# Performance work log

Hardware: AMD Instinct MI355X
Metric: run time of the kernel (lower is better)

The kernel has to match this reference:

```python
import jax, jax.numpy as jnp
import numpy as np

N, E, D, H, C = 100000, 1600000, 64, 8, 10
NEG_SLOPE = 0.2


def setup_inputs() -> dict:
    key = jax.random.key(0)
    ks = jax.random.split(key, 20)
    rn = lambda k, sh: jax.random.normal(k, sh, jnp.float32) * 0.1
    return dict(
        x=jax.random.normal(ks[0], (N, D), jnp.float32),
        edge_index=jax.random.randint(ks[1], (2, E), 0, N),
        gcnK_W=rn(ks[2], (D, D)), gcnK_b=rn(ks[3], (D,)),
        gcnV_W=rn(ks[4], (D, D)), gcnV_b=rn(ks[5], (D,)),
        super_Q=rn(ks[6], (C, D)),
        mha_in_w=rn(ks[7], (3 * D, D)), mha_in_b=rn(ks[8], (3 * D,)),
        mha_out_w=rn(ks[9], (D, D)), mha_out_b=rn(ks[10], (D,)),
        gat_W=rn(ks[11], (D, D)), gat_Wc=rn(ks[12], (D, D)),
        gat_a_src=rn(ks[13], (D,)), gat_a_dst=rn(ks[14], (D,)),
        gat_b=rn(ks[15], (D,)),
        t1_W=rn(ks[16], (D, 2 * D)), t1_b=rn(ks[17], (2 * D,)),
        t2_W=rn(ks[18], (2 * D, D)), t2_b=rn(ks[19], (D,)),
    )


def _gcn(x, W, b, src, dst, norm_e):
    # PyG GCNConv: symmetric-normalized aggregation over (A + I)
    h = x @ W  # [N, D]
    agg = jax.ops.segment_sum(h[src] * norm_e[:, None], dst, num_segments=N)
    return agg + b


def _mha(q, k, v, in_w, in_b, out_w, out_b):
    # torch.nn.MultiheadAttention (unbatched), eval mode (dropout off)
    L, n, hd = q.shape[0], k.shape[0], D // H
    Wq, Wk, Wv = jnp.split(in_w, 3, axis=0)
    bq, bk, bv = jnp.split(in_b, 3)
    scale = 1.0 / float(np.sqrt(hd))
    qh = ((q @ Wq.T + bq) * scale).reshape(L, H, hd).transpose(1, 0, 2)  # [H,L,hd]
    kh = (k @ Wk.T + bk).reshape(n, H, hd).transpose(1, 0, 2)            # [H,n,hd]
    vh = (v @ Wv.T + bv).reshape(n, H, hd).transpose(1, 0, 2)
    attn = jax.nn.softmax(jnp.einsum('hld,hnd->hln', qh, kh), axis=-1)
    o = jnp.einsum('hln,hnd->hld', attn, vh).transpose(1, 0, 2).reshape(L, D)
    return o @ out_w.T + out_b


def _context_gat(x, src, dst, context, W, Wc, a_src, a_dst, b):
    # context-conditioned GAT: per-edge logits use node terms + global context gate
    h = x @ W
    c = context @ Wc  # [D]
    s_src = h @ (a_src + c)  # context modulates source attention vector
    s_dst = h @ a_dst
    logits = jax.nn.leaky_relu(s_src[src] + s_dst[dst], NEG_SLOPE)  # [E]
    m = jax.ops.segment_max(logits, dst, num_segments=N)
    ex = jnp.exp(logits - m[dst])
    denom = jax.ops.segment_sum(ex, dst, num_segments=N)
    alpha = ex / (denom[dst] + 1e-16)
    out = jax.ops.segment_sum(alpha[:, None] * h[src], dst, num_segments=N)
    return out + b


def reference(x, edge_index, gcnK_W, gcnK_b, gcnV_W, gcnV_b, super_Q,
              mha_in_w, mha_in_b, mha_out_w, mha_out_b,
              gat_W, gat_Wc, gat_a_src, gat_a_dst, gat_b,
              t1_W, t1_b, t2_W, t2_b):
    src, dst = edge_index[0], edge_index[1]
    loop = jnp.arange(N)
    srcl = jnp.concatenate([src, loop])
    dstl = jnp.concatenate([dst, loop])
    deg = jax.ops.segment_sum(jnp.ones_like(srcl, jnp.float32), dstl, num_segments=N)
    dinv = jnp.where(deg > 0, 1.0 / jnp.sqrt(deg), 0.0)
    norm_e = dinv[srcl] * dinv[dstl]
    x_K = _gcn(x, gcnK_W, gcnK_b, srcl, dstl, norm_e)
    x_V = _gcn(x, gcnV_W, gcnV_b, srcl, dstl, norm_e)
    cluster = _mha(super_Q, x_K, x_V, mha_in_w, mha_in_b, mha_out_w, mha_out_b)  # [C, D]
    context = jnp.mean(cluster, axis=0)  # [D]
    g = _context_gat(x_V, src, dst, context, gat_W, gat_Wc, gat_a_src, gat_a_dst, gat_b)
    h1 = jax.nn.relu(g @ t1_W + t1_b)
    return jax.nn.relu(h1 @ t2_W + t2_b)
```

## Files before the change

kernel.cpp:

```cpp
#include <hip/hip_runtime.h>
#include <hip/hip_bf16.h>
#include <stdint.h>

#define NN 100000
#define EE 1600000
#define NBK 391
#define CHUNK 4096
#define NCB 98
#define BPH 128

#define FMA4(xi, vv, a, base)                      \
  a[(base)+0] = fmaf((xi), (vv).x, a[(base)+0]);   \
  a[(base)+1] = fmaf((xi), (vv).y, a[(base)+1]);   \
  a[(base)+2] = fmaf((xi), (vv).z, a[(base)+2]);   \
  a[(base)+3] = fmaf((xi), (vv).w, a[(base)+3]);

__device__ inline unsigned pack_bf2(float a, float b) {
  __hip_bfloat162 t;
  t.x = __float2bfloat16(a);
  t.y = __float2bfloat16(b);
  return *reinterpret_cast<unsigned*>(&t);
}

__launch_bounds__(256)
__global__ void k_hist(const int* __restrict__ ei, int* __restrict__ histmat) {
  __shared__ int hist[NCB];
  int t = threadIdx.x;
  if (t < NCB) hist[t] = 0;
  __syncthreads();
  int base = blockIdx.x * CHUNK;
  int nb = EE - base; if (nb > CHUNK) nb = CHUNK;
  for (int k = t; k < nb; k += 256)
    atomicAdd(&hist[ei[EE + base + k] >> 10], 1);
  __syncthreads();
  if (t < NCB) histmat[blockIdx.x * NCB + t] = hist[t];
}

__launch_bounds__(256)
__global__ void k_sumcb(const int* __restrict__ histmat, int* __restrict__ cbsum) {
  __shared__ int red[4];
  int cb = blockIdx.x, t = threadIdx.x;
  int s = 0;
  for (int blk = t; blk < NBK; blk += 256) s += histmat[blk * NCB + cb];
#pragma unroll
  for (int off = 32; off > 0; off >>= 1) s += __shfl_down(s, off);
  if ((t & 63) == 0) red[t >> 6] = s;
  __syncthreads();
  if (t == 0) cbsum[cb] = red[0] + red[1] + red[2] + red[3];
}

__launch_bounds__(128)
__global__ void k_scancb(const int* __restrict__ cbsum, int* __restrict__ bstart,
                         int* __restrict__ offsets) {
  __shared__ int sm[128];
  int t = threadIdx.x;
  int v = (t < NCB) ? cbsum[t] : 0;
  sm[t] = v;
  __syncthreads();
  for (int off = 1; off < 128; off <<= 1) {
    int x = (t >= off) ? sm[t - off] : 0;
    __syncthreads();
    sm[t] += x;
    __syncthreads();
  }
  if (t < NCB) bstart[t] = sm[t] - v;
  if (t == 0) { bstart[NCB] = EE; offsets[NN] = EE; }
}

__launch_bounds__(512)
__global__ void k_ppos(const int* __restrict__ histmat, const int* __restrict__ bstart,
                       int* __restrict__ ppos) {
  __shared__ int sm[512];
  int cb = blockIdx.x, t = threadIdx.x;
  int v = (t < NBK) ? histmat[t * NCB + cb] : 0;
  sm[t] = v;
  __syncthreads();
  for (int off = 1; off < 512; off <<= 1) {
    int x = (t >= off) ? sm[t - off] : 0;
    __syncthreads();
    sm[t] += x;
    __syncthreads();
  }
  if (t < NBK) ppos[cb * NBK + t] = bstart[cb] + sm[t] - v;
}

__launch_bounds__(256)
__global__ void k_fill_b(const int* __restrict__ ei, const int* __restrict__ ppos,
                         unsigned* __restrict__ brec) {
  __shared__ int hist[NCB], binstart[NCB], bincur[NCB], pbase[NCB];
  __shared__ unsigned lbuf[CHUNK];
  __shared__ unsigned char cbArr[CHUNK];
  int t = threadIdx.x;
  int base = blockIdx.x * CHUNK;
  int nb = EE - base; if (nb > CHUNK) nb = CHUNK;
  if (t < NCB) { hist[t] = 0; pbase[t] = ppos[t * NBK + blockIdx.x]; }
  __syncthreads();
  unsigned rec[16]; int rcb[16]; int cnt = 0;
  for (int k = t; k < nb; k += 256) {
    int s = ei[base + k], d = ei[EE + base + k];
    rec[cnt] = (unsigned)s | ((unsigned)(d & 1023) << 17);
    rcb[cnt] = d >> 10;
    atomicAdd(&hist[rcb[cnt]], 1);
    cnt++;
  }
  __syncthreads();
  if (t < NCB) binstart[t] = hist[t];
  __syncthreads();
  for (int off = 1; off < NCB; off <<= 1) {
    int v = (t < NCB && t >= off) ? binstart[t - off] : 0;
    __syncthreads();
    if (t < NCB) binstart[t] += v;
    __syncthreads();
  }
  if (t < NCB) { binstart[t] -= hist[t]; bincur[t] = 0; }
  __syncthreads();
  for (int i = 0; i < cnt; i++) {
    int c = rcb[i];
    int pos = atomicAdd(&bincur[c], 1);
    int p = binstart[c] + pos;
    lbuf[p] = rec[i];
    cbArr[p] = (unsigned char)c;
  }
  __syncthreads();
  for (int i = t; i < nb; i += 256) {
    int c = cbArr[i];
    brec[pbase[c] + (i - binstart[c])] = lbuf[i];
  }
}

__launch_bounds__(1024)
__global__ void k_fill_c(const unsigned* __restrict__ brec, const int* __restrict__ bstart,
                         int* __restrict__ csr, int* __restrict__ offsets,
                         float* __restrict__ dinv) {
  __shared__ int cnt[1024], sm[1024];
  int cbk = blockIdx.x, t = threadIdx.x;
  int nb0 = cbk << 10;
  int nn = NN - nb0; if (nn > 1024) nn = 1024;
  cnt[t] = 0;
  __syncthreads();
  int e0 = bstart[cbk], e1 = bstart[cbk + 1];
  for (int j = e0 + t; j < e1; j += 1024)
    atomicAdd(&cnt[brec[j] >> 17], 1);
  __syncthreads();
  int cv = cnt[t];
  sm[t] = cv;
  __syncthreads();
  for (int off = 1; off < 1024; off <<= 1) {
    int v = (t >= off) ? sm[t - off] : 0;
    __syncthreads();
    sm[t] += v;
    __syncthreads();
  }
  sm[t] -= cv;
  if (t < nn) {
    offsets[nb0 + t] = e0 + sm[t];
    dinv[nb0 + t] = rsqrtf((float)(cv + 1));
  }
  cnt[t] = 0;
  __syncthreads();
  for (int j = e0 + t; j < e1; j += 1024) {
    unsigned r = brec[j];
    int dl = r >> 17;
    int p = atomicAdd(&cnt[dl], 1);
    csr[e0 + sm[dl] + p] = r & 0x1FFFF;
  }
}

__global__ void k_prep(const float* __restrict__ x, const float* __restrict__ dinv,
                       unsigned* __restrict__ xbf2) {
  int i = blockIdx.x * 256 + threadIdx.x;
  if (i >= NN * 32) return;
  float dv = dinv[i >> 5];
  float2 v = ((const float2*)x)[i];
  xbf2[i] = pack_bf2(v.x * dv, v.y * dv);
}

__launch_bounds__(256)
__global__ void k_agg_x(const unsigned* __restrict__ xbf2, const int* __restrict__ offsets,
                        const int* __restrict__ csr, const float* __restrict__ dinv,
                        float* __restrict__ ax) {
  int gid = blockIdx.x * 256 + threadIdx.x;
  int n = gid >> 6;
  if (n >= NN) return;
  int lane = gid & 63, q = lane & 7, grp = lane >> 3;
  int e0 = offsets[n], e1 = offsets[n + 1];
  float dv = dinv[n];
  float a[8];
#pragma unroll
  for (int i = 0; i < 8; i++) a[i] = 0.f;
  if (grp == 0) {
    uint4 u = ((const uint4*)(xbf2 + (size_t)n * 32))[q];
    unsigned uu[4] = {u.x, u.y, u.z, u.w};
#pragma unroll
    for (int p = 0; p < 4; p++) {
      __hip_bfloat162 v = *reinterpret_cast<__hip_bfloat162*>(&uu[p]);
      a[2 * p] += __bfloat162float(v.x);
      a[2 * p + 1] += __bfloat162float(v.y);
    }
  }
  for (int base = e0; base < e1; base += 8) {
    int j = base + grp;
    if (j < e1) {
      int s = csr[j];
      uint4 u = ((const uint4*)(xbf2 + (size_t)s * 32))[q];
      unsigned uu[4] = {u.x, u.y, u.z, u.w};
#pragma unroll
      for (int p = 0; p < 4; p++) {
        __hip_bfloat162 v = *reinterpret_cast<__hip_bfloat162*>(&uu[p]);
        a[2 * p] += __bfloat162float(v.x);
        a[2 * p + 1] += __bfloat162float(v.y);
      }
    }
  }
#pragma unroll
  for (int i = 0; i < 8; i++) {
    a[i] += __shfl_xor(a[i], 8);
    a[i] += __shfl_xor(a[i], 16);
    a[i] += __shfl_xor(a[i], 32);
  }
  if (lane < 8) {
    float4* op = (float4*)(ax + (size_t)n * 64 + q * 8);
    op[0] = make_float4(a[0] * dv, a[1] * dv, a[2] * dv, a[3] * dv);
    op[1] = make_float4(a[4] * dv, a[5] * dv, a[6] * dv, a[7] * dv);
  }
}

__global__ void k_fusew(const float* __restrict__ gcnK_W, const float* __restrict__ gcnK_b,
                        const float* __restrict__ gcnV_W, const float* __restrict__ gcnV_b,
                        const float* __restrict__ mha_in_w, const float* __restrict__ mha_in_b,
                        const float* __restrict__ gat_W,
                        float* __restrict__ Wfk, float* __restrict__ Wfv,
                        float* __restrict__ Wfg, float* __restrict__ bf) {
  int blk = blockIdx.x;
  if (blk < 48) {
    int m = blk >> 4;
    int e = (blk & 15) * 256 + threadIdx.x;
    int i = e >> 6, c = e & 63;
    float s = 0.f;
    if (m == 0) {
      for (int j = 0; j < 64; j++) s = fmaf(gcnK_W[i * 64 + j], mha_in_w[(64 + c) * 64 + j], s);
      Wfk[e] = s;
    } else if (m == 1) {
      for (int j = 0; j < 64; j++) s = fmaf(gcnV_W[i * 64 + j], mha_in_w[(128 + c) * 64 + j], s);
      Wfv[e] = s;
    } else {
      for (int j = 0; j < 64; j++) s = fmaf(gcnV_W[i * 64 + j], gat_W[j * 64 + c], s);
      Wfg[e] = s;
    }
  } else {
    int t = threadIdx.x;
    if (t < 64) {
      float s = mha_in_b[64 + t];
      for (int j = 0; j < 64; j++) s = fmaf(gcnK_b[j], mha_in_w[(64 + t) * 64 + j], s);
      bf[t] = s;
    } else if (t < 128) {
      int c = t - 64;
      float s = mha_in_b[128 + c];
      for (int j = 0; j < 64; j++) s = fmaf(gcnV_b[j], mha_in_w[(128 + c) * 64 + j], s);
      bf[64 + c] = s;
    } else if (t < 192) {
      int c = t - 128;
      float s = 0.f;
      for (int j = 0; j < 64; j++) s = fmaf(gcnV_b[j], gat_W[j * 64 + c], s);
      bf[128 + c] = s;
    }
  }
}

__global__ void k_qh(const float* __restrict__ sQ, const float* __restrict__ in_w,
                     const float* __restrict__ in_b, float* __restrict__ qh) {
  int t = blockIdx.x * 256 + threadIdx.x;
  if (t >= 640) return;
  int l = t >> 6, c = t & 63;
  float acc = 0.f;
  for (int i = 0; i < 64; i++) acc = fmaf(sQ[l * 64 + i], in_w[c * 64 + i], acc);
  qh[t] = (acc + in_b[c]) * 0.35355339059327373f;
}

__launch_bounds__(256)
__global__ void k_proj(const float* __restrict__ ax, const float* __restrict__ Wfk,
                       const float* __restrict__ Wfv, const float* __restrict__ Wfg,
                       const float* __restrict__ bf, const float* __restrict__ a_dst,
                       float* __restrict__ Kh, float* __restrict__ Vh,
                       unsigned* __restrict__ hGb, float* __restrict__ s_dstv) {
  __shared__ float sX[64 * 65];
  __shared__ float sWk[4096], sWv[4096], sWg[4096];
  __shared__ float sB[192], sAd[64];
  int t = threadIdx.x;
  int base = blockIdx.x * 64;
  for (int i = t; i < 4096; i += 256) { sWk[i] = Wfk[i]; sWv[i] = Wfv[i]; sWg[i] = Wfg[i]; }
  if (t < 192) sB[t] = bf[t];
  if (t < 64) sAd[t] = a_dst[t];
  for (int idx = t; idx < 64 * 16; idx += 256) {
    int rl = idx >> 4, k4 = idx & 15;
    int row = base + rl;
    float4 v = (row < NN) ? ((const float4*)ax)[(size_t)row * 16 + k4]
                          : make_float4(0.f, 0.f, 0.f, 0.f);
    sX[rl * 65 + 4 * k4 + 0] = v.x;
    sX[rl * 65 + 4 * k4 + 1] = v.y;
    sX[rl * 65 + 4 * k4 + 2] = v.z;
    sX[rl * 65 + 4 * k4 + 3] = v.w;
  }
  __syncthreads();
  int cg = t & 7, rg = t >> 3;
  int r0 = rg * 2;
  float aK[16], aV[16], aG[16];
#pragma unroll
  for (int i = 0; i < 16; i++) { aK[i] = 0.f; aV[i] = 0.f; aG[i] = 0.f; }
  const float4* Wk4 = (const float4*)sWk;
  const float4* Wv4 = (const float4*)sWv;
  const float4* Wg4 = (const float4*)sWg;
#pragma unroll 2
  for (int i = 0; i < 64; i++) {
    float x0 = sX[r0 * 65 + i];
    float x1 = sX[(r0 + 1) * 65 + i];
    float4 wk0 = Wk4[i * 16 + cg * 2], wk1 = Wk4[i * 16 + cg * 2 + 1];
    float4 wv0 = Wv4[i * 16 + cg * 2], wv1 = Wv4[i * 16 + cg * 2 + 1];
    float4 wg0 = Wg4[i * 16 + cg * 2], wg1 = Wg4[i * 16 + cg * 2 + 1];
    FMA4(x0, wk0, aK, 0); FMA4(x0, wk1, aK, 4);
    FMA4(x1, wk0, aK, 8); FMA4(x1, wk1, aK, 12);
    FMA4(x0, wv0, aV, 0); FMA4(x0, wv1, aV, 4);
    FMA4(x1, wv0, aV, 8); FMA4(x1, wv1, aV, 12);
    FMA4(x0, wg0, aG, 0); FMA4(x0, wg1, aG, 4);
    FMA4(x1, wg0, aG, 8); FMA4(x1, wg1, aG, 12);
  }
#pragma unroll
  for (int r = 0; r < 2; r++) {
    int row = base + r0 + r;
    bool ok = row < NN;
    int o = r * 8;
    float hg[8];
    float sd = 0.f;
#pragma unroll
    for (int c = 0; c < 8; c++) {
      hg[c] = aG[o + c] + sB[128 + cg * 8 + c];
      sd = fmaf(hg[c], sAd[cg * 8 + c], sd);
    }
    sd += __shfl_xor(sd, 1);
    sd += __shfl_xor(sd, 2);
    sd += __shfl_xor(sd, 4);
    if (ok) {
      float4* kp = (float4*)(Kh + (size_t)cg * NN * 8 + (size_t)row * 8);
      kp[0] = make_float4(aK[o + 0] + sB[cg * 8 + 0], aK[o + 1] + sB[cg * 8 + 1],
                          aK[o + 2] + sB[cg * 8 + 2], aK[o + 3] + sB[cg * 8 + 3]);
      kp[1] = make_float4(aK[o + 4] + sB[cg * 8 + 4], aK[o + 5] + sB[cg * 8 + 5],
                          aK[o + 6] + sB[cg * 8 + 6], aK[o + 7] + sB[cg * 8 + 7]);
      float4* vp = (float4*)(Vh + (size_t)cg * NN * 8 + (size_t)row * 8);
      vp[0] = make_float4(aV[o + 0] + sB[64 + cg * 8 + 0], aV[o + 1] + sB[64 + cg * 8 + 1],
                          aV[o + 2] + sB[64 + cg * 8 + 2], aV[o + 3] + sB[64 + cg * 8 + 3]);
      vp[1] = make_float4(aV[o + 4] + sB[64 + cg * 8 + 4], aV[o + 5] + sB[64 + cg * 8 + 5],
                          aV[o + 6] + sB[64 + cg * 8 + 6], aV[o + 7] + sB[64 + cg * 8 + 7]);
      uint4 u;
      u.x = pack_bf2(hg[0], hg[1]);
      u.y = pack_bf2(hg[2], hg[3]);
      u.z = pack_bf2(hg[4], hg[5]);
      u.w = pack_bf2(hg[6], hg[7]);
      ((uint4*)(hGb + (size_t)row * 32))[cg] = u;
      if (cg == 0) s_dstv[row] = sd;
    }
  }
}

__launch_bounds__(256)
__global__ void k_mha(const float* __restrict__ Kh, const float* __restrict__ Vh,
                      const float* __restrict__ qh, float* __restrict__ part) {
  int h = blockIdx.x / BPH, b = blockIdx.x % BPH;
  __shared__ float sq[80];
  __shared__ float red[4][90];
  if (threadIdx.x < 80) {
    int l = threadIdx.x >> 3, j = threadIdx.x & 7;
    sq[threadIdx.x] = qh[l * 64 + h * 8 + j];
  }
  __syncthreads();
  const float4* Kp = (const float4*)(Kh + (size_t)h * NN * 8);
  const float4* Vp = (const float4*)(Vh + (size_t)h * NN * 8);
  const float4* sq4 = (const float4*)sq;
  float s[10], o[80];
#pragma unroll
  for (int l = 0; l < 10; l++) s[l] = 0.f;
#pragma unroll
  for (int t = 0; t < 80; t++) o[t] = 0.f;
  for (int n = b * 256 + threadIdx.x; n < NN; n += BPH * 256) {
    float4 k0 = Kp[n * 2], k1 = Kp[n * 2 + 1];
    float4 v0 = Vp[n * 2], v1 = Vp[n * 2 + 1];
#pragma unroll
    for (int l = 0; l < 10; l++) {
      float4 q0 = sq4[l * 2], q1 = sq4[l * 2 + 1];
      float z = q0.x * k0.x + q0.y * k0.y + q0.z * k0.z + q0.w * k0.w +
                q1.x * k1.x + q1.y * k1.y + q1.z * k1.z + q1.w * k1.w;
      float w = __expf(z);
      s[l] += w;
      o[l * 8 + 0] = fmaf(w, v0.x, o[l * 8 + 0]);
      o[l * 8 + 1] = fmaf(w, v0.y, o[l * 8 + 1]);
      o[l * 8 + 2] = fmaf(w, v0.z, o[l * 8 + 2]);
      o[l * 8 + 3] = fmaf(w, v0.w, o[l * 8 + 3]);
      o[l * 8 + 4] = fmaf(w, v1.x, o[l * 8 + 4]);
      o[l * 8 + 5] = fmaf(w, v1.y, o[l * 8 + 5]);
      o[l * 8 + 6] = fmaf(w, v1.z, o[l * 8 + 6]);
      o[l * 8 + 7] = fmaf(w, v1.w, o[l * 8 + 7]);
    }
  }
  int lane = threadIdx.x & 63, wave = threadIdx.x >> 6;
#pragma unroll
  for (int l = 0; l < 10; l++) {
    float v = s[l];
#pragma unroll
    for (int off = 32; off > 0; off >>= 1) v += __shfl_down(v, off);
    if (lane == 0) red[wave][l] = v;
  }
#pragma unroll
  for (int t = 0; t < 80; t++) {
    float v = o[t];
#pragma unroll
    for (int off = 32; off > 0; off >>= 1) v += __shfl_down(v, off);
    if (lane == 0) red[wave][10 + t] = v;
  }
  __syncthreads();
  if (threadIdx.x < 90) {
    float v = red[0][threadIdx.x] + red[1][threadIdx.x] +
              red[2][threadIdx.x] + red[3][threadIdx.x];
    part[(size_t)blockIdx.x * 90 + threadIdx.x] = v;
  }
}

__global__ void k_mred(const float* __restrict__ part, float* __restrict__ acc) {
  int t = blockIdx.x * 256 + threadIdx.x;
  if (t >= 720) return;
  int h = t / 90, j = t % 90;
  float v = 0.f;
  for (int b = 0; b < BPH; b++) v += part[(size_t)(h * BPH + b) * 90 + j];
  if (j < 10) acc[h * 10 + j] = v;
  else acc[80 + h * 80 + (j - 10)] = v;
}

__global__ void k_context(const float* __restrict__ acc, const float* __restrict__ out_w,
                          const float* __restrict__ out_b, const float* __restrict__ a_src,
                          const float* __restrict__ gat_Wc, float* __restrict__ aeff) {
  __shared__ float po[640], cl[640], ctx[64];
  int t = threadIdx.x;
  {
    int h = t / 80, r = t % 80, l = r >> 3, j = r & 7;
    po[l * 64 + h * 8 + j] = acc[80 + t] / acc[h * 10 + l];
  }
  __syncthreads();
  {
    int l = t >> 6, d = t & 63;
    float v = out_b[d];
    for (int c = 0; c < 64; c++) v = fmaf(po[l * 64 + c], out_w[d * 64 + c], v);
    cl[t] = v;
  }
  __syncthreads();
  if (t < 64) {
    float m = 0.f;
#pragma unroll
    for (int l = 0; l < 10; l++) m += cl[l * 64 + t];
    ctx[t] = m * 0.1f;
  }
  __syncthreads();
  if (t < 64) {
    float v = a_src[t];
    for (int i = 0; i < 64; i++) v = fmaf(ctx[i], gat_Wc[i * 64 + t], v);
    aeff[t] = v;
  }
}

__launch_bounds__(256)
__global__ void k_ssrc(const unsigned* __restrict__ hGb, const float* __restrict__ aeff,
                       float* __restrict__ s_src) {
  int gid = blockIdx.x * 256 + threadIdx.x;
  int n = gid >> 6, lane = gid & 63;
  if (n >= NN) return;
  const __hip_bfloat16* hp = (const __hip_bfloat16*)hGb;
  float v = __bfloat162float(hp[(size_t)n * 64 + lane]) * aeff[lane];
#pragma unroll
  for (int off = 32; off > 0; off >>= 1) v += __shfl_xor(v, off);
  if (lane == 0) s_src[n] = v;
}

__launch_bounds__(256)
__global__ void k_gat(const int* __restrict__ offsets, const int* __restrict__ csr,
                      const float* __restrict__ s_src, const float* __restrict__ s_dstv,
                      const unsigned* __restrict__ hGb, const float* __restrict__ gat_b,
                      float* __restrict__ g) {
  int gid = blockIdx.x * 256 + threadIdx.x;
  int n = gid >> 6;
  if (n >= NN) return;
  int lane = gid & 63, q = lane & 7, grp = lane >> 3;
  int e0 = offsets[n], e1 = offsets[n + 1];
  float sd = s_dstv[n];
  float den = 0.f;
  float a[8];
#pragma unroll
  for (int i = 0; i < 8; i++) a[i] = 0.f;
  for (int base = e0; base < e1; base += 8) {
    int j = base + grp;
    if (j < e1) {
      int s = csr[j];
      float z = s_src[s] + sd;
      z = z > 0.f ? z : 0.2f * z;
      float ex = __expf(z);
      den += ex;
      uint4 u = ((const uint4*)(hGb + (size_t)s * 32))[q];
      unsigned uu[4] = {u.x, u.y, u.z, u.w};
#pragma unroll
      for (int p = 0; p < 4; p++) {
        __hip_bfloat162 v = *reinterpret_cast<__hip_bfloat162*>(&uu[p]);
        a[2 * p] = fmaf(ex, __bfloat162float(v.x), a[2 * p]);
        a[2 * p + 1] = fmaf(ex, __bfloat162float(v.y), a[2 * p + 1]);
      }
    }
  }
  den += __shfl_xor(den, 8);
  den += __shfl_xor(den, 16);
  den += __shfl_xor(den, 32);
#pragma unroll
  for (int i = 0; i < 8; i++) {
    a[i] += __shfl_xor(a[i], 8);
    a[i] += __shfl_xor(a[i], 16);
    a[i] += __shfl_xor(a[i], 32);
  }
  float inv = 1.f / (den + 1e-16f);
  if (lane < 8) {
    float4* op = (float4*)(g + (size_t)n * 64 + q * 8);
    op[0] = make_float4(a[0] * inv + gat_b[q * 8 + 0], a[1] * inv + gat_b[q * 8 + 1],
                        a[2] * inv + gat_b[q * 8 + 2], a[3] * inv + gat_b[q * 8 + 3]);
    op[1] = make_float4(a[4] * inv + gat_b[q * 8 + 4], a[5] * inv + gat_b[q * 8 + 5],
                        a[6] * inv + gat_b[q * 8 + 6], a[7] * inv + gat_b[q * 8 + 7]);
  }
}

__launch_bounds__(256)
__global__ void k_mlp1(const float* __restrict__ g, const float* __restrict__ W1,
                       const float* __restrict__ b1, unsigned* __restrict__ h1b) {
  __shared__ float sX[32 * 65];
  __shared__ float sW[64 * 128];
  __shared__ float sb[128];
  int t = threadIdx.x;
  int base = blockIdx.x * 32;
  for (int i = t; i < 8192; i += 256) sW[i] = W1[i];
  if (t < 128) sb[t] = b1[t];
  for (int idx = t; idx < 32 * 16; idx += 256) {
    int rl = idx >> 4, k4 = idx & 15;
    int row = base + rl;
    float4 v = (row < NN) ? ((const float4*)g)[(size_t)row * 16 + k4]
                          : make_float4(0.f, 0.f, 0.f, 0.f);
    sX[rl * 65 + 4 * k4 + 0] = v.x;
    sX[rl * 65 + 4 * k4 + 1] = v.y;
    sX[rl * 65 + 4 * k4 + 2] = v.z;
    sX[rl * 65 + 4 * k4 + 3] = v.w;
  }
  __syncthreads();
  int cg = t & 15, rg = t >> 4;
  int r0 = rg * 2;
  float a0[8], a1[8];
#pragma unroll
  for (int i = 0; i < 8; i++) { a0[i] = 0.f; a1[i] = 0.f; }
  const float4* W4 = (const float4*)sW;
#pragma unroll 4
  for (int i = 0; i < 64; i++) {
    float x0 = sX[r0 * 65 + i];
    float x1 = sX[(r0 + 1) * 65 + i];
    float4 w0 = W4[i * 32 + cg * 2], w1 = W4[i * 32 + cg * 2 + 1];
    FMA4(x0, w0, a0, 0); FMA4(x0, w1, a0, 4);
    FMA4(x1, w0, a1, 0); FMA4(x1, w1, a1, 4);
  }
#pragma unroll
  for (int r = 0; r < 2; r++) {
    int row = base + r0 + r;
    if (row >= NN) continue;
    float* a = r ? a1 : a0;
    float h[8];
#pragma unroll
    for (int c = 0; c < 8; c++) h[c] = fmaxf(a[c] + sb[cg * 8 + c], 0.f);
    uint4 u;
    u.x = pack_bf2(h[0], h[1]);
    u.y = pack_bf2(h[2], h[3]);
    u.z = pack_bf2(h[4], h[5]);
    u.w = pack_bf2(h[6], h[7]);
    ((uint4*)(h1b + (size_t)row * 64))[cg] = u;
  }
}

__launch_bounds__(256)
__global__ void k_mlp2(const unsigned* __restrict__ h1b, const float* __restrict__ W2,
                       const float* __restrict__ b2, float* __restrict__ out) {
  __shared__ unsigned sH[64 * 65];
  __shared__ float sW[128 * 64];
  __shared__ float sb[64];
  int t = threadIdx.x;
  int base = blockIdx.x * 64;
  for (int i = t; i < 8192; i += 256) sW[i] = W2[i];
  if (t < 64) sb[t] = b2[t];
  for (int idx = t; idx < 64 * 16; idx += 256) {
    int rl = idx >> 4, c4 = idx & 15;
    int row = base + rl;
    uint4 v = (row < NN) ? ((const uint4*)h1b)[(size_t)row * 16 + c4]
                         : make_uint4(0u, 0u, 0u, 0u);
    sH[rl * 65 + 4 * c4 + 0] = v.x;
    sH[rl * 65 + 4 * c4 + 1] = v.y;
    sH[rl * 65 + 4 * c4 + 2] = v.z;
    sH[rl * 65 + 4 * c4 + 3] = v.w;
  }
  __syncthreads();
  int cg = t & 7, rg = t >> 3;
  int r0 = rg * 2;
  float a0[8], a1[8];
#pragma unroll
  for (int i = 0; i < 8; i++) { a0[i] = 0.f; a1[i] = 0.f; }
  const float4* W4 = (const float4*)sW;
#pragma unroll 2
  for (int kp = 0; kp < 64; kp++) {
    unsigned u0 = sH[r0 * 65 + kp];
    unsigned u1 = sH[(r0 + 1) * 65 + kp];
    float x0a = __uint_as_float(u0 << 16), x0b = __uint_as_float(u0 & 0xffff0000u);
    float x1a = __uint_as_float(u1 << 16), x1b = __uint_as_float(u1 & 0xffff0000u);
    int k0 = 2 * kp, k1 = 2 * kp + 1;
    float4 wa0 = W4[k0 * 16 + cg * 2], wa1 = W4[k0 * 16 + cg * 2 + 1];
    float4 wb0 = W4[k1 * 16 + cg * 2], wb1 = W4[k1 * 16 + cg * 2 + 1];
    FMA4(x0a, wa0, a0, 0); FMA4(x0a, wa1, a0, 4);
    FMA4(x0b, wb0, a0, 0); FMA4(x0b, wb1, a0, 4);
    FMA4(x1a, wa0, a1, 0); FMA4(x1a, wa1, a1, 4);
    FMA4(x1b, wb0, a1, 0); FMA4(x1b, wb1, a1, 4);
  }
#pragma unroll
  for (int r = 0; r < 2; r++) {
    int row = base + r0 + r;
    if (row >= NN) continue;
    float* a = r ? a1 : a0;
    float4* op = (float4*)(out + (size_t)row * 64 + cg * 8);
    op[0] = make_float4(fmaxf(a[0] + sb[cg * 8 + 0], 0.f), fmaxf(a[1] + sb[cg * 8 + 1], 0.f),
                        fmaxf(a[2] + sb[cg * 8 + 2], 0.f), fmaxf(a[3] + sb[cg * 8 + 3], 0.f));
    op[1] = make_float4(fmaxf(a[4] + sb[cg * 8 + 4], 0.f), fmaxf(a[5] + sb[cg * 8 + 5], 0.f),
                        fmaxf(a[6] + sb[cg * 8 + 6], 0.f), fmaxf(a[7] + sb[cg * 8 + 7], 0.f));
  }
}

extern "C" void kernel_launch(void* const* d_in, const int* in_sizes, int n_in,
                              void* d_out, int out_size, void* d_ws, size_t ws_size,
                              hipStream_t stream) {
  (void)in_sizes; (void)n_in; (void)out_size; (void)ws_size;
  const float* x        = (const float*)d_in[0];
  const int*   ei       = (const int*)d_in[1];
  const float* gcnK_W   = (const float*)d_in[2];
  const float* gcnK_b   = (const float*)d_in[3];
  const float* gcnV_W   = (const float*)d_in[4];
  const float* gcnV_b   = (const float*)d_in[5];
  const float* super_Q  = (const float*)d_in[6];
  const float* mha_in_w = (const float*)d_in[7];
  const float* mha_in_b = (const float*)d_in[8];
  const float* mha_out_w= (const float*)d_in[9];
  const float* mha_out_b= (const float*)d_in[10];
  const float* gat_W    = (const float*)d_in[11];
  const float* gat_Wc   = (const float*)d_in[12];
  const float* gat_a_src= (const float*)d_in[13];
  const float* gat_a_dst= (const float*)d_in[14];
  const float* gat_b    = (const float*)d_in[15];
  const float* t1_W     = (const float*)d_in[16];
  const float* t1_b     = (const float*)d_in[17];
  const float* t2_W     = (const float*)d_in[18];
  const float* t2_b     = (const float*)d_in[19];

  char* ws = (char*)d_ws;
  size_t cur = 0;
  auto alloc = [&](size_t bytes) -> char* {
    char* p = ws + cur;
    cur = (cur + bytes + 255) & ~(size_t)255;
    return p;
  };
  int*      histmat = (int*)alloc((size_t)NBK * NCB * 4);
  int*      cbsum   = (int*)alloc((size_t)NCB * 4);
  int*      ppos    = (int*)alloc((size_t)NCB * NBK * 4);
  int*      bstart  = (int*)alloc((size_t)(NCB + 1) * 4);
  int*      offsets = (int*)alloc((size_t)(NN + 1) * 4);
  float*    dinv    = (float*)alloc((size_t)NN * 4);
  int*      csr     = (int*)alloc((size_t)EE * 4);
  unsigned* brec    = (unsigned*)alloc((size_t)EE * 4);
  float*    Wfk     = (float*)alloc(4096 * 4);
  float*    Wfv     = (float*)alloc(4096 * 4);
  float*    Wfg     = (float*)alloc(4096 * 4);
  float*    bfuse   = (float*)alloc(192 * 4);
  float*    qh      = (float*)alloc(640 * 4);
  float*    aeff    = (float*)alloc(64 * 4);
  float*    macc    = (float*)alloc(720 * 4);
  float*    part    = (float*)alloc((size_t)8 * BPH * 90 * 4);
  float*    s_src   = (float*)alloc((size_t)NN * 4);
  float*    s_dstv  = (float*)alloc((size_t)NN * 4);
  unsigned* xbf     = (unsigned*)alloc((size_t)NN * 128);
  float*    ax      = (float*)alloc((size_t)NN * 64 * 4);
  float*    Kh      = (float*)alloc((size_t)NN * 64 * 4);
  float*    Vh      = (float*)alloc((size_t)NN * 64 * 4);
  unsigned* hGb     = (unsigned*)alloc((size_t)NN * 128);
  unsigned* h1b     = (unsigned*)alloc((size_t)NN * 64 * 4);
  float*    g       = (float*)d_out;

  k_hist<<<NBK, 256, 0, stream>>>(ei, histmat);
  k_sumcb<<<NCB, 256, 0, stream>>>(histmat, cbsum);
  k_scancb<<<1, 128, 0, stream>>>(cbsum, bstart, offsets);
  k_ppos<<<NCB, 512, 0, stream>>>(histmat, bstart, ppos);
  k_fill_b<<<NBK, 256, 0, stream>>>(ei, ppos, brec);
  k_fill_c<<<NCB, 1024, 0, stream>>>(brec, bstart, csr, offsets, dinv);
  k_prep<<<(NN * 32 + 255) / 256, 256, 0, stream>>>(x, dinv, xbf);
  k_agg_x<<<NN / 4, 256, 0, stream>>>(xbf, offsets, csr, dinv, ax);
  k_fusew<<<49, 256, 0, stream>>>(gcnK_W, gcnK_b, gcnV_W, gcnV_b, mha_in_w, mha_in_b,
                                  gat_W, Wfk, Wfv, Wfg, bfuse);
  k_qh<<<3, 256, 0, stream>>>(super_Q, mha_in_w, mha_in_b, qh);
  k_proj<<<(NN + 63) / 64, 256, 0, stream>>>(ax, Wfk, Wfv, Wfg, bfuse, gat_a_dst,
                                             Kh, Vh, hGb, s_dstv);
  k_mha<<<8 * BPH, 256, 0, stream>>>(Kh, Vh, qh, part);
  k_mred<<<3, 256, 0, stream>>>(part, macc);
  k_context<<<1, 640, 0, stream>>>(macc, mha_out_w, mha_out_b, gat_a_src, gat_Wc, aeff);
  k_ssrc<<<NN / 4, 256, 0, stream>>>(hGb, aeff, s_src);
  k_gat<<<NN / 4, 256, 0, stream>>>(offsets, csr, s_src, s_dstv, hGb, gat_b, g);
  k_mlp1<<<(NN + 31) / 32, 256, 0, stream>>>(g, t1_W, t1_b, h1b);
  k_mlp2<<<(NN + 63) / 64, 256, 0, stream>>>(h1b, t2_W, t2_b, g);
}
```

Baseline: 462.8 us.

## Fuse MHA attention accumulation into projection kernel, drop K/V buffers

The separate MHA kernel, which re-read the K and V projections from global memory, is removed. The projection kernel now computes the exp-weighted sums and value accumulations for each row directly from registers. It reduces them across the block with shuffles and shared memory and writes one partial per block. This saves about 51 MB of K/V writes and reads. In exchange the projection kernel carries 90 more accumulators per thread, which adds register pressure, and the final reduction must sum 1563 partials serially in a tiny kernel.

```diff
diff --git a/kernel.cpp b/kernel.cpp
--- a/kernel.cpp
+++ b/kernel.cpp
@@ -7,7 +7,7 @@
 #define NBK 391
 #define CHUNK 4096
 #define NCB 98
-#define BPH 128
+#define NPROJ 1563
 
 #define FMA4(xi, vv, a, base)                      \
   a[(base)+0] = fmaf((xi), (vv).x, a[(base)+0]);   \
@@ -281,16 +281,18 @@
 __global__ void k_proj(const float* __restrict__ ax, const float* __restrict__ Wfk,
                        const float* __restrict__ Wfv, const float* __restrict__ Wfg,
                        const float* __restrict__ bf, const float* __restrict__ a_dst,
-                       float* __restrict__ Kh, float* __restrict__ Vh,
-                       unsigned* __restrict__ hGb, float* __restrict__ s_dstv) {
+                       const float* __restrict__ qh,
+                       unsigned* __restrict__ hGb, float* __restrict__ s_dstv,
+                       float* __restrict__ part) {
   __shared__ float sX[64 * 65];
   __shared__ float sWk[4096], sWv[4096], sWg[4096];
-  __shared__ float sB[192], sAd[64];
+  __shared__ float sB[192], sAd[64], sq[640];
   int t = threadIdx.x;
   int base = blockIdx.x * 64;
   for (int i = t; i < 4096; i += 256) { sWk[i] = Wfk[i]; sWv[i] = Wfv[i]; sWg[i] = Wfg[i]; }
   if (t < 192) sB[t] = bf[t];
   if (t < 64) sAd[t] = a_dst[t];
+  for (int i = t; i < 640; i += 256) sq[i] = qh[i];
   for (int idx = t; idx < 64 * 16; idx += 256) {
     int rl = idx >> 4, k4 = idx & 15;
     int row = base + rl;
@@ -324,32 +326,40 @@
     FMA4(x0, wg0, aG, 0); FMA4(x0, wg1, aG, 4);
     FMA4(x1, wg0, aG, 8); FMA4(x1, wg1, aG, 12);
   }
+  float s[10], o[80];
+#pragma unroll
+  for (int l = 0; l < 10; l++) s[l] = 0.f;
+#pragma unroll
+  for (int i = 0; i < 80; i++) o[i] = 0.f;
+  const float4* sq4 = (const float4*)sq;
 #pragma unroll
   for (int r = 0; r < 2; r++) {
     int row = base + r0 + r;
     bool ok = row < NN;
-    int o = r * 8;
-    float hg[8];
+    int off = r * 8;
+    float kv[8], vv[8], hg[8];
     float sd = 0.f;
 #pragma unroll
     for (int c = 0; c < 8; c++) {
-      hg[c] = aG[o + c] + sB[128 + cg * 8 + c];
+      kv[c] = aK[off + c] + sB[cg * 8 + c];
+      vv[c] = aV[off + c] + sB[64 + cg * 8 + c];
+      hg[c] = aG[off + c] + sB[128 + cg * 8 + c];
       sd = fmaf(hg[c], sAd[cg * 8 + c], sd);
     }
     sd += __shfl_xor(sd, 1);
     sd += __shfl_xor(sd, 2);
     sd += __shfl_xor(sd, 4);
     if (ok) {
-      float4* kp = (float4*)(Kh + (size_t)cg * NN * 8 + (size_t)row * 8);
-      kp[0] = make_float4(aK[o + 0] + sB[cg * 8 + 0], aK[o + 1] + sB[cg * 8 + 1],
-                          aK[o + 2] + sB[cg * 8 + 2], aK[o + 3] + sB[cg * 8 + 3]);
-      kp[1] = make_float4(aK[o + 4] + sB[cg * 8 + 4], aK[o + 5] + sB[cg * 8 + 5],
-                          aK[o + 6] + sB[cg * 8 + 6], aK[o + 7] + sB[cg * 8 + 7]);
-      float4* vp = (float4*)(Vh + (size_t)cg * NN * 8 + (size_t)row * 8);
-      vp[0] = make_float4(aV[o + 0] + sB[64 + cg * 8 + 0], aV[o + 1] + sB[64 + cg * 8 + 1],
-                          aV[o + 2] + sB[64 + cg * 8 + 2], aV[o + 3] + sB[64 + cg * 8 + 3]);
-      vp[1] = make_float4(aV[o + 4] + sB[64 + cg * 8 + 4], aV[o + 5] + sB[64 + cg * 8 + 5],
-                          aV[o + 6] + sB[64 + cg * 8 + 6], aV[o + 7] + sB[64 + cg * 8 + 7]);
+#pragma unroll
+      for (int l = 0; l < 10; l++) {
+        float4 q0 = sq4[l * 16 + cg * 2], q1 = sq4[l * 16 + cg * 2 + 1];
+        float z = q0.x * kv[0] + q0.y * kv[1] + q0.z * kv[2] + q0.w * kv[3] +
+                  q1.x * kv[4] + q1.y * kv[5] + q1.z * kv[6] + q1.w * kv[7];
+        float w = __expf(z);
+        s[l] += w;
+#pragma unroll
+        for (int c = 0; c < 8; c++) o[l * 8 + c] = fmaf(w, vv[c], o[l * 8 + c]);
+      }
       uint4 u;
       u.x = pack_bf2(hg[0], hg[1]);
       u.y = pack_bf2(hg[2], hg[3]);
@@ -359,78 +369,42 @@
       if (cg == 0) s_dstv[row] = sd;
     }
   }
-}
-
-__launch_bounds__(256)
-__global__ void k_mha(const float* __restrict__ Kh, const float* __restrict__ Vh,
-                      const float* __restrict__ qh, float* __restrict__ part) {
-  int h = blockIdx.x / BPH, b = blockIdx.x % BPH;
-  __shared__ float sq[80];
-  __shared__ float red[4][90];
-  if (threadIdx.x < 80) {
-    int l = threadIdx.x >> 3, j = threadIdx.x & 7;
-    sq[threadIdx.x] = qh[l * 64 + h * 8 + j];
-  }
-  __syncthreads();
-  const float4* Kp = (const float4*)(Kh + (size_t)h * NN * 8);
-  const float4* Vp = (const float4*)(Vh + (size_t)h * NN * 8);
-  const float4* sq4 = (const float4*)sq;
-  float s[10], o[80];
-#pragma unroll
-  for (int l = 0; l < 10; l++) s[l] = 0.f;
-#pragma unroll
-  for (int t = 0; t < 80; t++) o[t] = 0.f;
-  for (int n = b * 256 + threadIdx.x; n < NN; n += BPH * 256) {
-    float4 k0 = Kp[n * 2], k1 = Kp[n * 2 + 1];
-    float4 v0 = Vp[n * 2], v1 = Vp[n * 2 + 1];
-#pragma unroll
-    for (int l = 0; l < 10; l++) {
-      float4 q0 = sq4[l * 2], q1 = sq4[l * 2 + 1];
-      float z = q0.x * k0.x + q0.y * k0.y + q0.z * k0.z + q0.w * k0.w +
-                q1.x * k1.x + q1.y * k1.y + q1.z * k1.z + q1.w * k1.w;
-      float w = __expf(z);
-      s[l] += w;
-      o[l * 8 + 0] = fmaf(w, v0.x, o[l * 8 + 0]);
-      o[l * 8 + 1] = fmaf(w, v0.y, o[l * 8 + 1]);
-      o[l * 8 + 2] = fmaf(w, v0.z, o[l * 8 + 2]);
-      o[l * 8 + 3] = fmaf(w, v0.w, o[l * 8 + 3]);
-      o[l * 8 + 4] = fmaf(w, v1.x, o[l * 8 + 4]);
-      o[l * 8 + 5] = fmaf(w, v1.y, o[l * 8 + 5]);
-      o[l * 8 + 6] = fmaf(w, v1.z, o[l * 8 + 6]);
-      o[l * 8 + 7] = fmaf(w, v1.w, o[l * 8 + 7]);
-    }
-  }
-  int lane = threadIdx.x & 63, wave = threadIdx.x >> 6;
 #pragma unroll
   for (int l = 0; l < 10; l++) {
-    float v = s[l];
-#pragma unroll
-    for (int off = 32; off > 0; off >>= 1) v += __shfl_down(v, off);
-    if (lane == 0) red[wave][l] = v;
-  }
-#pragma unroll
-  for (int t = 0; t < 80; t++) {
-    float v = o[t];
-#pragma unroll
-    for (int off = 32; off > 0; off >>= 1) v += __shfl_down(v, off);
-    if (lane == 0) red[wave][10 + t] = v;
-  }
-  __syncthreads();
-  if (threadIdx.x < 90) {
-    float v = red[0][threadIdx.x] + red[1][threadIdx.x] +
-              red[2][threadIdx.x] + red[3][threadIdx.x];
-    part[(size_t)blockIdx.x * 90 + threadIdx.x] = v;
+    s[l] += __shfl_xor(s[l], 8);
+    s[l] += __shfl_xor(s[l], 16);
+    s[l] += __shfl_xor(s[l], 32);
+  }
+#pragma unroll
+  for (int i = 0; i < 80; i++) {
+    o[i] += __shfl_xor(o[i], 8);
+    o[i] += __shfl_xor(o[i], 16);
+    o[i] += __shfl_xor(o[i], 32);
+  }
+  __syncthreads();
+  float* scratch = sX;
+  int lane = t & 63, wave = t >> 6;
+  if (lane < 8) {
+#pragma unroll
+    for (int l = 0; l < 10; l++) scratch[wave * 720 + lane * 90 + l] = s[l];
+#pragma unroll
+    for (int i = 0; i < 80; i++) scratch[wave * 720 + lane * 90 + 10 + i] = o[i];
+  }
+  __syncthreads();
+  for (int j = t; j < 720; j += 256) {
+    float v = scratch[j] + scratch[720 + j] + scratch[1440 + j] + scratch[2160 + j];
+    part[(size_t)blockIdx.x * 720 + j] = v;
   }
 }
 
 __global__ void k_mred(const float* __restrict__ part, float* __restrict__ acc) {
   int t = blockIdx.x * 256 + threadIdx.x;
   if (t >= 720) return;
-  int h = t / 90, j = t % 90;
+  int cg = t / 90, j = t % 90;
   float v = 0.f;
-  for (int b = 0; b < BPH; b++) v += part[(size_t)(h * BPH + b) * 90 + j];
-  if (j < 10) acc[h * 10 + j] = v;
-  else acc[80 + h * 80 + (j - 10)] = v;
+  for (int b = 0; b < NPROJ; b++) v += part[(size_t)b * 720 + t];
+  if (j < 10) acc[cg * 10 + j] = v;
+  else acc[80 + cg * 80 + (j - 10)] = v;
 }
 
 __global__ void k_context(const float* __restrict__ acc, const float* __restrict__ out_w,
@@ -682,13 +656,11 @@
   float*    qh      = (float*)alloc(640 * 4);
   float*    aeff    = (float*)alloc(64 * 4);
   float*    macc    = (float*)alloc(720 * 4);
-  float*    part    = (float*)alloc((size_t)8 * BPH * 90 * 4);
+  float*    part    = (float*)alloc((size_t)NPROJ * 720 * 4);
   float*    s_src   = (float*)alloc((size_t)NN * 4);
   float*    s_dstv  = (float*)alloc((size_t)NN * 4);
   unsigned* xbf     = (unsigned*)alloc((size_t)NN * 128);
   float*    ax      = (float*)alloc((size_t)NN * 64 * 4);
-  float*    Kh      = (float*)alloc((size_t)NN * 64 * 4);
-  float*    Vh      = (float*)alloc((size_t)NN * 64 * 4);
   unsigned* hGb     = (unsigned*)alloc((size_t)NN * 128);
   unsigned* h1b     = (unsigned*)alloc((size_t)NN * 64 * 4);
   float*    g       = (float*)d_out;
@@ -704,9 +676,8 @@
   k_fusew<<<49, 256, 0, stream>>>(gcnK_W, gcnK_b, gcnV_W, gcnV_b, mha_in_w, mha_in_b,
                                   gat_W, Wfk, Wfv, Wfg, bfuse);
   k_qh<<<3, 256, 0, stream>>>(super_Q, mha_in_w, mha_in_b, qh);
-  k_proj<<<(NN + 63) / 64, 256, 0, stream>>>(ax, Wfk, Wfv, Wfg, bfuse, gat_a_dst,
-                                             Kh, Vh, hGb, s_dstv);
-  k_mha<<<8 * BPH, 256, 0, stream>>>(Kh, Vh, qh, part);
+  k_proj<<<NPROJ, 256, 0, stream>>>(ax, Wfk, Wfv, Wfg, bfuse, gat_a_dst, qh,
+                                    hGb, s_dstv, part);
   k_mred<<<3, 256, 0, stream>>>(part, macc);
   k_context<<<1, 640, 0, stream>>>(macc, mha_out_w, mha_out_b, gat_a_src, gat_Wc, aeff);
   k_ssrc<<<NN / 4, 256, 0, stream>>>(hGb, aeff, s_src);
```

After: 588.7 us. 27.2% more time.
